# Kernel optimization log

Measured on AMD Instinct MI355X. Metric: run time of the kernel, lower is better.

Reference implementation:

```python
import jax, jax.numpy as jnp
import numpy as np

N = 20000      # nodes
E = 320000     # edges (before self-loops)
IN = 128       # in_channels
D = 256        # hidden_channels (d_model)
H = 8          # nhead
DH = D // H    # d_head
L = 2          # num_layers
B = 64         # NUM_DEGREE_BUCKETS
DFF = 2 * D    # dim_ff = d*2 per source


def setup_inputs() -> dict:
    key = jax.random.key(0)
    ks = jax.random.split(key, 24)
    w = lambda k, s: (jax.random.normal(k, s, jnp.float32) * 0.02)
    x = jax.random.normal(ks[0], (N, IN), jnp.float32)
    row = jax.random.randint(ks[1], (E,), 0, N, jnp.int32)
    col = jax.random.randint(ks[2], (E,), 0, N, jnp.int32)
    deg_emb = w(ks[3], (B, D)).at[0].set(0.0)  # padding_idx=0
    return dict(
        x=x, row=row, col=col,
        Wx=w(ks[4], (IN, D)), bx=jnp.zeros((D,), jnp.float32),
        deg_emb=deg_emb,
        sb=w(ks[5], (L, B, H)),
        Wq=w(ks[6], (L, D, D)), bq=jnp.zeros((L, D), jnp.float32),
        Wk=w(ks[7], (L, D, D)), bk=jnp.zeros((L, D), jnp.float32),
        Wv=w(ks[8], (L, D, D)), bv=jnp.zeros((L, D), jnp.float32),
        Wo=w(ks[9], (L, D, D)), bo=jnp.zeros((L, D), jnp.float32),
        ln1_g=jnp.ones((L, D), jnp.float32), ln1_b=jnp.zeros((L, D), jnp.float32),
        ln2_g=jnp.ones((L, D), jnp.float32), ln2_b=jnp.zeros((L, D), jnp.float32),
        W1=w(ks[10], (L, D, DFF)), b1=jnp.zeros((L, DFF), jnp.float32),
        W2=w(ks[11], (L, DFF, D)), b2=jnp.zeros((L, D), jnp.float32),
    )


def _ln(x, g, b):
    m = x.mean(-1, keepdims=True)
    v = ((x - m) ** 2).mean(-1, keepdims=True)
    return (x - m) / jnp.sqrt(v + 1e-5) * g + b


def reference(x, row, col, Wx, bx, deg_emb, sb, Wq, bq, Wk, bk, Wv, bv, Wo, bo,
              ln1_g, ln1_b, ln2_g, ln2_b, W1, b1, W2, b2):
    n = x.shape[0]
    # degree from original adjacency (before self loops)
    deg = jax.ops.segment_sum(jnp.ones_like(row, jnp.float32), row, num_segments=n)
    bucket = jnp.clip(jnp.floor(jnp.log2(jnp.maximum(deg, 1.0))), 1, B - 1).astype(jnp.int32)
    h = x @ Wx + bx + deg_emb[bucket]
    # set_diag(): append self loops
    sl = jnp.arange(n, dtype=row.dtype)
    r = jnp.concatenate([row, sl])
    c = jnp.concatenate([col, sl])
    scale = DH ** -0.5
    for i in range(L):
        Q = (h @ Wq[i] + bq[i]).reshape(n, H, DH)
        K = (h @ Wk[i] + bk[i]).reshape(n, H, DH)
        V = (h @ Wv[i] + bv[i]).reshape(n, H, DH)
        # per-edge multi-head scores + degree-bucket spatial bias  [E_tot, H]
        scores = (Q[r] * K[c]).sum(-1) * scale + sb[i][bucket[r]] + sb[i][bucket[c]]
        mx = jax.ops.segment_max(scores, r, num_segments=n)
        es = jnp.exp(scores - mx[r])
        ss = jax.ops.segment_sum(es, r, num_segments=n)
        alpha = es / jnp.maximum(ss[r], 1e-12)
        agg = jax.ops.segment_sum(alpha[:, :, None] * V[c], r, num_segments=n).reshape(n, D)
        out = agg @ Wo[i] + bo[i]
        h = _ln(h + out, ln1_g[i], ln1_b[i])
        ff = jax.nn.gelu(h @ W1[i] + b1[i], approximate=False) @ W2[i] + b2[i]
        h = _ln(h + ff, ln2_g[i], ln2_b[i])
    return h
```

## Files before the change

kernel.cpp:

```cpp
#include <hip/hip_runtime.h>
#include <hip/hip_bf16.h>
#include <math.h>

#define NNODES 20000
#define NPAD   20096
#define NEDGES 320000
#define INC 128
#define DMODEL 256
#define NHEAD 8
#define DHEAD 32
#define NLAYER 2
#define NBUCKET 64
#define DFF 512
#define ETOT (NEDGES + NNODES)
#define UNR 8

typedef __attribute__((ext_vector_type(8))) short short8v;
typedef __attribute__((ext_vector_type(4))) float f32x4;

__device__ __forceinline__ float bf2f(unsigned short u) {
    return __uint_as_float(((unsigned int)u) << 16);
}
__device__ __forceinline__ unsigned short f2bf(float f) {
    unsigned int u = __float_as_uint(f);
    unsigned int r = (u + 0x7FFFu + ((u >> 16) & 1u)) >> 16;
    return (unsigned short)r;
}
__device__ __forceinline__ void gl16(const unsigned short* g, unsigned short* l) {
    __builtin_amdgcn_global_load_lds(
        (const __attribute__((address_space(1))) void*)g,
        (__attribute__((address_space(3))) void*)l, 16, 0, 0);
}

__global__ void count_deg_k(const int* __restrict__ row, int* __restrict__ deg, int E) {
    int e = blockIdx.x * 256 + threadIdx.x;
    if (e < E) atomicAdd(&deg[row[e]], 1);
}

__global__ __launch_bounds__(1024) void scan_offsets_k(const int* __restrict__ deg,
                                                       int* __restrict__ off,
                                                       int* __restrict__ cur,
                                                       int* __restrict__ bkt, int n) {
    const int T = 1024;
    int t = threadIdx.x;
    int chunk = (n + T - 1) / T;
    int base = t * chunk;
    int s = 0;
    for (int i = 0; i < chunk; ++i) {
        int idx = base + i;
        if (idx < n) {
            int d = deg[idx];
            int dd = d < 1 ? 1 : d;
            int b = 31 - __clz(dd);
            bkt[idx] = min(max(b, 1), NBUCKET - 1);
            s += d + 1;
        }
    }
    __shared__ int ps[1024];
    ps[t] = s;
    __syncthreads();
    for (int d = 1; d < T; d <<= 1) {
        int v = (t >= d) ? ps[t - d] : 0;
        __syncthreads();
        ps[t] += v;
        __syncthreads();
    }
    int run = (t == 0) ? 0 : ps[t - 1];
    for (int i = 0; i < chunk; ++i) {
        int idx = base + i;
        if (idx < n) {
            off[idx] = run; cur[idx] = run;
            run += deg[idx] + 1;
        }
    }
    if (t == T - 1) off[n] = ps[T - 1];
}

__global__ void csr_fill_k(const int* __restrict__ row, const int* __restrict__ col,
                           const int* __restrict__ bkt,
                           int* __restrict__ cur, int* __restrict__ csr, int E, int n) {
    int e = blockIdx.x * 256 + threadIdx.x;
    if (e < E) {
        int c = col[e];
        int p = atomicAdd(&cur[row[e]], 1);
        csr[p] = c | (bkt[c] << 19);
    } else if (e < E + n) {
        int nn = e - E;
        int p = atomicAdd(&cur[nn], 1);
        csr[p] = nn | (bkt[nn] << 19);
    }
}

__global__ void cvt_bf16_k(const float* __restrict__ s, unsigned short* __restrict__ d, int n) {
    int i = (blockIdx.x * 256 + threadIdx.x) * 4;
    if (i < n) {
        float4 v = *(const float4*)(s + i);
        ushort4 o;
        o.x = f2bf(v.x); o.y = f2bf(v.y); o.z = f2bf(v.z); o.w = f2bf(v.w);
        *(ushort4*)(d + i) = o;
    }
}

struct TDesc { const float* src; unsigned short* dst; int K; int N; int tileStart; };
struct TPack { TDesc d[13]; int nd; };

__global__ __launch_bounds__(256) void mega_transpose_k(TPack p) {
    __shared__ float tile[32][33];
    const int tb = blockIdx.x;
    int di = 0;
    for (int i = 1; i < 13; ++i)
        if (i < p.nd && p.d[i].tileStart <= tb) di = i;
    const float* __restrict__ src = p.d[di].src;
    unsigned short* __restrict__ dst = p.d[di].dst;
    const int K = p.d[di].K, N = p.d[di].N;
    const int local = tb - p.d[di].tileStart;
    const int tpn = N >> 5;
    const int n0 = (local % tpn) * 32;
    const int k0 = (local / tpn) * 32;
    const int t = threadIdx.x;
    {
        int r = t >> 3, c = (t & 7) * 4;
        float4 v = *(const float4*)(src + (size_t)(k0 + r) * N + n0 + c);
        tile[r][c] = v.x; tile[r][c + 1] = v.y; tile[r][c + 2] = v.z; tile[r][c + 3] = v.w;
    }
    __syncthreads();
    {
        int n = t >> 3, k = (t & 7) * 4;
        ushort4 o;
        o.x = f2bf(tile[k][n]); o.y = f2bf(tile[k + 1][n]);
        o.z = f2bf(tile[k + 2][n]); o.w = f2bf(tile[k + 3][n]);
        *(ushort4*)(dst + (size_t)(n0 + n) * K + k0 + k) = o;
    }
}

__global__ void concat_bias2_k(const float* __restrict__ bq, const float* __restrict__ bk,
                               const float* __restrict__ bv,
                               float* __restrict__ d0, float* __restrict__ d1) {
    int t = blockIdx.x * 256 + threadIdx.x;
    int l = t / 768, u = t - l * 768;
    float v;
    if (u < 256) v = bq[l * DMODEL + u];
    else if (u < 512) v = bk[l * DMODEL + u - 256];
    else v = bv[l * DMODEL + u - 512];
    (l ? d1 : d0)[u] = v;
}

__global__ __launch_bounds__(256) void gemm_bf16_k(
        const unsigned short* __restrict__ A, const unsigned short* __restrict__ Wt,
        const float* __restrict__ bias,
        float* __restrict__ Cf, unsigned short* __restrict__ Cb,
        int M, int K, int Nout,
        const float* __restrict__ emb, const int* __restrict__ bkt, int act) {
    __shared__ unsigned short As[128 * 32];
    __shared__ unsigned short Bs[128 * 32];
    const int bm = blockIdx.x * 128;
    const int bn = blockIdx.y * 128;
    const int t = threadIdx.x;
    const int wid = t >> 6, lane = t & 63;
    const int wm = wid >> 1, wn = wid & 1;
    const int l16 = lane & 15, kslc = lane >> 4;
    const int srow = lane >> 2, scol = (lane & 3) * 8;

    f32x4 acc[4][4] = {};

    for (int k0 = 0; k0 < K; k0 += 32) {
        const unsigned short* gA = A + (size_t)(bm + wid * 32 + srow) * K + k0 + scol;
        const unsigned short* gB = Wt + (size_t)(bn + wid * 32 + srow) * K + k0 + scol;
        gl16(gA,          &As[(wid * 32) * 32]);
        gl16(gA + 16 * K, &As[(wid * 32 + 16) * 32]);
        gl16(gB,          &Bs[(wid * 32) * 32]);
        gl16(gB + 16 * K, &Bs[(wid * 32 + 16) * 32]);
        __syncthreads();
        short8v a[4], b[4];
        #pragma unroll
        for (int f = 0; f < 4; ++f) {
            a[f] = *(const short8v*)(&As[(wm * 64 + f * 16 + l16) * 32 + kslc * 8]);
            b[f] = *(const short8v*)(&Bs[(wn * 64 + f * 16 + l16) * 32 + kslc * 8]);
        }
        #pragma unroll
        for (int fm = 0; fm < 4; ++fm)
            #pragma unroll
            for (int fn = 0; fn < 4; ++fn)
                acc[fm][fn] = __builtin_amdgcn_mfma_f32_16x16x32_bf16(
                    a[fm], b[fn], acc[fm][fn], 0, 0, 0);
        __syncthreads();
    }

    #pragma unroll
    for (int fm = 0; fm < 4; ++fm) {
        #pragma unroll
        for (int fn = 0; fn < 4; ++fn) {
            int cc = wn * 64 + fn * 16 + l16;
            int gn = bn + cc;
            float bn_v = bias[gn];
            int rbase = bm + wm * 64 + fm * 16 + (lane >> 4) * 4;
            #pragma unroll
            for (int r = 0; r < 4; ++r) {
                int gm = rbase + r;
                if (gm >= M) continue;
                float v = acc[fm][fn][r] + bn_v;
                if (emb) v += emb[(size_t)bkt[gm] * Nout + gn];
                if (act) v = 0.5f * v * (1.f + erff(v * 0.70710678118654752f));
                if (Cf) Cf[(size_t)gm * Nout + gn] = v;
                if (Cb) Cb[(size_t)gm * Nout + gn] = f2bf(v);
            }
        }
    }
}


#define LOADB(CC, KK, VV, SB, J)                                               \
    do {                                                                        \
        _Pragma("unroll")                                                       \
        for (int e = 0; e < UNR; ++e)                                           \
            CC[e] = csr[min((J) + e, s1 - 1)];                                  \
        _Pragma("unroll")                                                       \
        for (int e = 0; e < UNR; ++e) {                                         \
            const unsigned short* base =                                        \
                QKV + (size_t)(CC[e] & 0x7FFFF) * 768 + hh * 32 + d2 * 2;       \
            KK[e] = *(const ushort2*)(base + 256);                              \
            VV[e] = *(const ushort2*)(base + 512);                              \
            SB[e] = sb_i[(CC[e] >> 19) * NHEAD + hh];                           \
        }                                                                       \
    } while (0)

#define COMPUTE(KK, VV, SB, J)                                                 \
    do {                                                                        \
        _Pragma("unroll")                                                       \
        for (int e = 0; e < UNR; ++e) {                                         \
            float p = qx * bf2f(KK[e].x) + qy * bf2f(KK[e].y);                  \
            _Pragma("unroll")                                                   \
            for (int mk = 8; mk >= 1; mk >>= 1) p += __shfl_xor(p, mk);         \
            float sc = p * scale + sbn + SB[e];                                 \
            if ((J) + e < s1) {                                                 \
                float mn = fmaxf(m, sc);                                        \
                float corr = __expf(m - mn);                                    \
                float es = __expf(sc - mn);                                     \
                s = s * corr + es;                                              \
                ax = ax * corr + es * bf2f(VV[e].x);                            \
                ay = ay * corr + es * bf2f(VV[e].y);                            \
                m = mn;                                                         \
            }                                                                   \
        }                                                                       \
    } while (0)

__global__ __launch_bounds__(128) void attn_bf16_k(
        const unsigned short* __restrict__ QKV,
        const int* __restrict__ off, const int* __restrict__ csr,
        const int* __restrict__ bkt, const float* __restrict__ sb_i,
        unsigned short* __restrict__ aggb) {
    const int node = blockIdx.x;
    const int t = threadIdx.x;
    const int hh = t >> 4, d2 = t & 15;
    const int s0 = off[node], s1 = off[node + 1];
    const ushort2 q2 = *(const ushort2*)(QKV + (size_t)node * 768 + hh * 32 + d2 * 2);
    const float qx = bf2f(q2.x), qy = bf2f(q2.y);
    const float sbn = sb_i[bkt[node] * NHEAD + hh];
    const float scale = 0.17677669529663689f;
    float m = -1e30f, s = 0.f, ax = 0.f, ay = 0.f;

    int ccA[UNR]; ushort2 kkA[UNR], vvA[UNR]; float sbA[UNR];
    int ccB[UNR]; ushort2 kkB[UNR], vvB[UNR]; float sbB[UNR];

    LOADB(ccA, kkA, vvA, sbA, s0);
    for (int j = s0; j < s1; j += 2 * UNR) {
        LOADB(ccB, kkB, vvB, sbB, j + UNR);
        COMPUTE(kkA, vvA, sbA, j);
        LOADB(ccA, kkA, vvA, sbA, j + 2 * UNR);
        COMPUTE(kkB, vvB, sbB, j + UNR);
    }

    float inv = 1.f / fmaxf(s, 1e-12f);
    ushort2 o;
    o.x = f2bf(ax * inv); o.y = f2bf(ay * inv);
    *(ushort2*)(aggb + (size_t)node * DMODEL + hh * 32 + d2 * 2) = o;
}

__global__ __launch_bounds__(256) void add_ln_k(float* __restrict__ h,
                                                const float* __restrict__ add,
                                                const float* __restrict__ g,
                                                const float* __restrict__ b,
                                                unsigned short* __restrict__ hb) {
    const int r = blockIdx.x;
    const int t = threadIdx.x;
    float x = h[(size_t)r * DMODEL + t] + add[(size_t)r * DMODEL + t];
    __shared__ float red[4];
    float s = x;
    #pragma unroll
    for (int mk = 32; mk >= 1; mk >>= 1) s += __shfl_xor(s, mk);
    if ((t & 63) == 0) red[t >> 6] = s;
    __syncthreads();
    float mean = (red[0] + red[1] + red[2] + red[3]) * (1.f / DMODEL);
    float dx = x - mean;
    __syncthreads();
    float v = dx * dx;
    #pragma unroll
    for (int mk = 32; mk >= 1; mk >>= 1) v += __shfl_xor(v, mk);
    if ((t & 63) == 0) red[t >> 6] = v;
    __syncthreads();
    float var = (red[0] + red[1] + red[2] + red[3]) * (1.f / DMODEL);
    float y = dx * rsqrtf(var + 1e-5f) * g[t] + b[t];
    h[(size_t)r * DMODEL + t] = y;
    hb[(size_t)r * DMODEL + t] = f2bf(y);
}

extern "C" void kernel_launch(void* const* d_in, const int* in_sizes, int n_in,
                              void* d_out, int out_size, void* d_ws, size_t ws_size,
                              hipStream_t stream) {
    const float* x      = (const float*)d_in[0];
    const int*   row    = (const int*)d_in[1];
    const int*   col    = (const int*)d_in[2];
    const float* Wx     = (const float*)d_in[3];
    const float* bx     = (const float*)d_in[4];
    const float* degemb = (const float*)d_in[5];
    const float* sb     = (const float*)d_in[6];
    const float* Wq     = (const float*)d_in[7];
    const float* bq     = (const float*)d_in[8];
    const float* Wk     = (const float*)d_in[9];
    const float* bk     = (const float*)d_in[10];
    const float* Wv     = (const float*)d_in[11];
    const float* bv     = (const float*)d_in[12];
    const float* Wo     = (const float*)d_in[13];
    const float* bo     = (const float*)d_in[14];
    const float* ln1g   = (const float*)d_in[15];
    const float* ln1b   = (const float*)d_in[16];
    const float* ln2g   = (const float*)d_in[17];
    const float* ln2b   = (const float*)d_in[18];
    const float* W1     = (const float*)d_in[19];
    const float* b1     = (const float*)d_in[20];
    const float* W2     = (const float*)d_in[21];
    const float* b2     = (const float*)d_in[22];

    const int Nn = NNODES, E = NEDGES;
    float* h = (float*)d_out;

    char* w = (char*)d_ws;
    unsigned short* hb   = (unsigned short*)w; w += (size_t)NPAD * DMODEL * 2;
    unsigned short* QKVb = (unsigned short*)w; w += (size_t)Nn * 768 * 2;
    unsigned short* AGGb = (unsigned short*)w; w += (size_t)NPAD * DMODEL * 2;
    unsigned short* FFb  = (unsigned short*)w; w += (size_t)NPAD * DFF * 2;
    float*          OUT  = (float*)w;          w += (size_t)Nn * DMODEL * 4;
    unsigned short* xb   = (unsigned short*)w; w += (size_t)NPAD * INC * 2;
    unsigned short* Wxt  = (unsigned short*)w; w += (size_t)DMODEL * INC * 2;
    unsigned short* Wqkvt[NLAYER]; float* bqkv[NLAYER];
    unsigned short *Wot[NLAYER], *W1t[NLAYER], *W2t[NLAYER];
    for (int l = 0; l < NLAYER; ++l) {
        Wqkvt[l] = (unsigned short*)w; w += (size_t)768 * DMODEL * 2;
        bqkv[l]  = (float*)w;          w += 768 * 4;
        Wot[l]   = (unsigned short*)w; w += (size_t)DMODEL * DMODEL * 2;
        W1t[l]   = (unsigned short*)w; w += (size_t)DFF * DMODEL * 2;
        W2t[l]   = (unsigned short*)w; w += (size_t)DMODEL * DFF * 2;
    }
    int* CSR = (int*)w; w += (size_t)ETOT * 4;
    int* OFF = (int*)w; w += (Nn + 1) * 4;
    int* CUR = (int*)w; w += Nn * 4;
    int* DEG = (int*)w; w += Nn * 4;
    int* BKT = (int*)w; w += Nn * 4;

    hipMemsetAsync(DEG, 0, Nn * sizeof(int), stream);
    count_deg_k<<<(E + 255) / 256, 256, 0, stream>>>(row, DEG, E);
    scan_offsets_k<<<1, 1024, 0, stream>>>(DEG, OFF, CUR, BKT, Nn);
    csr_fill_k<<<(E + Nn + 255) / 256, 256, 0, stream>>>(row, col, BKT, CUR, CSR, E, Nn);

    cvt_bf16_k<<<((size_t)Nn * INC / 4 + 255) / 256, 256, 0, stream>>>(x, xb, Nn * INC);
    {
        TPack pk; int nd = 0, tt = 0;
        auto add = [&](const float* s, unsigned short* d, int K, int N) {
            pk.d[nd].src = s; pk.d[nd].dst = d; pk.d[nd].K = K; pk.d[nd].N = N;
            pk.d[nd].tileStart = tt;
            tt += (K / 32) * (N / 32);
            ++nd;
        };
        const size_t DD = (size_t)DMODEL * DMODEL;
        add(Wx, Wxt, INC, DMODEL);
        for (int l = 0; l < NLAYER; ++l) {
            add(Wq + l * DD, Wqkvt[l],                DMODEL, DMODEL);
            add(Wk + l * DD, Wqkvt[l] + 256 * DMODEL, DMODEL, DMODEL);
            add(Wv + l * DD, Wqkvt[l] + 512 * DMODEL, DMODEL, DMODEL);
            add(Wo + l * DD, Wot[l], DMODEL, DMODEL);
            add(W1 + (size_t)l * DMODEL * DFF, W1t[l], DMODEL, DFF);
            add(W2 + (size_t)l * DFF * DMODEL, W2t[l], DFF, DMODEL);
        }
        pk.nd = nd;
        mega_transpose_k<<<tt, 256, 0, stream>>>(pk);
        concat_bias2_k<<<6, 256, 0, stream>>>(bq, bk, bv, bqkv[0], bqkv[1]);
    }

    const int MB = (Nn + 127) / 128;

    {
        dim3 grid(MB, DMODEL / 128);
        gemm_bf16_k<<<grid, 256, 0, stream>>>(xb, Wxt, bx, h, hb, Nn, INC, DMODEL,
                                              degemb, BKT, 0);
    }

    for (int l = 0; l < NLAYER; ++l) {
        const float* sb_i = sb + (size_t)l * NBUCKET * NHEAD;
        dim3 gQKV(MB, 768 / 128);
        dim3 gD(MB, DMODEL / 128);
        dim3 gF(MB, DFF / 128);

        gemm_bf16_k<<<gQKV, 256, 0, stream>>>(hb, Wqkvt[l], bqkv[l], nullptr, QKVb,
                                              Nn, DMODEL, 768, nullptr, nullptr, 0);
        attn_bf16_k<<<Nn, 128, 0, stream>>>(QKVb, OFF, CSR, BKT, sb_i, AGGb);
        gemm_bf16_k<<<gD, 256, 0, stream>>>(AGGb, Wot[l], bo + (size_t)l * DMODEL,
                                            OUT, nullptr, Nn, DMODEL, DMODEL,
                                            nullptr, nullptr, 0);
        add_ln_k<<<Nn, 256, 0, stream>>>(h, OUT, ln1g + (size_t)l * DMODEL,
                                         ln1b + (size_t)l * DMODEL, hb);
        gemm_bf16_k<<<gF, 256, 0, stream>>>(hb, W1t[l], b1 + (size_t)l * DFF,
                                            nullptr, FFb, Nn, DMODEL, DFF,
                                            nullptr, nullptr, 1);
        gemm_bf16_k<<<gD, 256, 0, stream>>>(FFb, W2t[l], b2 + (size_t)l * DMODEL,
                                            OUT, nullptr, Nn, DFF, DMODEL,
                                            nullptr, nullptr, 0);
        add_ln_k<<<Nn, 256, 0, stream>>>(h, OUT, ln2g + (size_t)l * DMODEL,
                                         ln2b + (size_t)l * DMODEL, hb);
    }
}
```

Measured before the change: 638.1 us.

## Fuse output and FFN2 GEMMs with residual add and LayerNorm

Adds a 512-thread GEMM kernel in which each block covers a 128-row by full 256-column tile, so the residual add and LayerNorm can be computed in the epilogue through shuffles and a shared-memory reduction. It replaces the separate N=256 GEMMs and the per-row add_ln kernels, removing the fp32 OUT intermediate buffer and four launches per forward. The cost is a grid of only about 157 blocks, each with a larger register footprint, which may leave the GPU underoccupied.

```diff
diff --git a/kernel.cpp b/kernel.cpp
--- a/kernel.cpp
+++ b/kernel.cpp
@@ -203,6 +203,146 @@
                 if (act) v = 0.5f * v * (1.f + erff(v * 0.70710678118654752f));
                 if (Cf) Cf[(size_t)gm * Nout + gn] = v;
                 if (Cb) Cb[(size_t)gm * Nout + gn] = f2bf(v);
+            }
+        }
+    }
+}
+
+__global__ __launch_bounds__(512) void gemm_ln_k(
+        const unsigned short* __restrict__ A, const unsigned short* __restrict__ Wt,
+        const float* __restrict__ bias,
+        float* __restrict__ h, unsigned short* __restrict__ hb,
+        const float* __restrict__ lng, const float* __restrict__ lnb,
+        int M, int K) {
+    __shared__ unsigned short As[128 * 32];
+    __shared__ unsigned short Bs[256 * 32];
+    __shared__ float red[128 * 4];
+    const int bm = blockIdx.x * 128;
+    const int t = threadIdx.x;
+    const int wid = t >> 6, lane = t & 63;
+    const int wm = wid >> 2, wn = wid & 3;
+    const int l16 = lane & 15, kslc = lane >> 4;
+    const int srow = lane >> 2, scol = (lane & 3) * 8;
+
+    f32x4 acc[4][4] = {};
+
+    for (int k0 = 0; k0 < K; k0 += 32) {
+        if (wid < 4) {
+            const unsigned short* gA = A + (size_t)(bm + wid * 32 + srow) * K + k0 + scol;
+            gl16(gA,          &As[(wid * 32) * 32]);
+            gl16(gA + 16 * K, &As[(wid * 32 + 16) * 32]);
+        } else {
+            const int w4 = wid - 4;
+            const unsigned short* gB = Wt + (size_t)(w4 * 64 + srow) * K + k0 + scol;
+            gl16(gB,          &Bs[(w4 * 64) * 32]);
+            gl16(gB + 16 * K, &Bs[(w4 * 64 + 16) * 32]);
+            gl16(gB + 32 * K, &Bs[(w4 * 64 + 32) * 32]);
+            gl16(gB + 48 * K, &Bs[(w4 * 64 + 48) * 32]);
+        }
+        __syncthreads();
+        short8v a[4], bb[4];
+        #pragma unroll
+        for (int f = 0; f < 4; ++f) {
+            a[f]  = *(const short8v*)(&As[(wm * 64 + f * 16 + l16) * 32 + kslc * 8]);
+            bb[f] = *(const short8v*)(&Bs[(wn * 64 + f * 16 + l16) * 32 + kslc * 8]);
+        }
+        #pragma unroll
+        for (int fm = 0; fm < 4; ++fm)
+            #pragma unroll
+            for (int fn = 0; fn < 4; ++fn)
+                acc[fm][fn] = __builtin_amdgcn_mfma_f32_16x16x32_bf16(
+                    a[fm], bb[fn], acc[fm][fn], 0, 0, 0);
+        __syncthreads();
+    }
+
+    #pragma unroll
+    for (int fm = 0; fm < 4; ++fm) {
+        #pragma unroll
+        for (int fn = 0; fn < 4; ++fn) {
+            const int gn = wn * 64 + fn * 16 + l16;
+            const float bv = bias[gn];
+            #pragma unroll
+            for (int r = 0; r < 4; ++r) {
+                const int gm = bm + wm * 64 + fm * 16 + kslc * 4 + r;
+                float v = acc[fm][fn][r] + bv;
+                if (gm < M) v += h[(size_t)gm * DMODEL + gn];
+                acc[fm][fn][r] = v;
+            }
+        }
+    }
+
+    float mean[4][4];
+    #pragma unroll
+    for (int fm = 0; fm < 4; ++fm)
+        #pragma unroll
+        for (int r = 0; r < 4; ++r) {
+            float p = acc[fm][0][r] + acc[fm][1][r] + acc[fm][2][r] + acc[fm][3][r];
+            #pragma unroll
+            for (int mk = 8; mk >= 1; mk >>= 1) p += __shfl_xor(p, mk);
+            mean[fm][r] = p;
+        }
+    if (l16 == 0) {
+        #pragma unroll
+        for (int fm = 0; fm < 4; ++fm)
+            #pragma unroll
+            for (int r = 0; r < 4; ++r)
+                red[(wm * 64 + fm * 16 + kslc * 4 + r) * 4 + wn] = mean[fm][r];
+    }
+    __syncthreads();
+    #pragma unroll
+    for (int fm = 0; fm < 4; ++fm)
+        #pragma unroll
+        for (int r = 0; r < 4; ++r) {
+            const int lr = wm * 64 + fm * 16 + kslc * 4 + r;
+            mean[fm][r] = (red[lr * 4] + red[lr * 4 + 1] + red[lr * 4 + 2] + red[lr * 4 + 3])
+                          * (1.f / DMODEL);
+        }
+    __syncthreads();
+
+    float var[4][4];
+    #pragma unroll
+    for (int fm = 0; fm < 4; ++fm)
+        #pragma unroll
+        for (int r = 0; r < 4; ++r) {
+            const float mu = mean[fm][r];
+            float d0 = acc[fm][0][r] - mu, d1 = acc[fm][1][r] - mu;
+            float d2 = acc[fm][2][r] - mu, d3 = acc[fm][3][r] - mu;
+            float p = d0 * d0 + d1 * d1 + d2 * d2 + d3 * d3;
+            #pragma unroll
+            for (int mk = 8; mk >= 1; mk >>= 1) p += __shfl_xor(p, mk);
+            var[fm][r] = p;
+        }
+    if (l16 == 0) {
+        #pragma unroll
+        for (int fm = 0; fm < 4; ++fm)
+            #pragma unroll
+            for (int r = 0; r < 4; ++r)
+                red[(wm * 64 + fm * 16 + kslc * 4 + r) * 4 + wn] = var[fm][r];
+    }
+    __syncthreads();
+    #pragma unroll
+    for (int fm = 0; fm < 4; ++fm)
+        #pragma unroll
+        for (int r = 0; r < 4; ++r) {
+            const int lr = wm * 64 + fm * 16 + kslc * 4 + r;
+            var[fm][r] = (red[lr * 4] + red[lr * 4 + 1] + red[lr * 4 + 2] + red[lr * 4 + 3])
+                         * (1.f / DMODEL);
+        }
+
+    #pragma unroll
+    for (int fm = 0; fm < 4; ++fm) {
+        #pragma unroll
+        for (int r = 0; r < 4; ++r) {
+            const int gm = bm + wm * 64 + fm * 16 + kslc * 4 + r;
+            if (gm >= M) continue;
+            const float mu = mean[fm][r];
+            const float rs = rsqrtf(var[fm][r] + 1e-5f);
+            #pragma unroll
+            for (int fn = 0; fn < 4; ++fn) {
+                const int gn = wn * 64 + fn * 16 + l16;
+                float y = (acc[fm][fn][r] - mu) * rs * lng[gn] + lnb[gn];
+                h[(size_t)gm * DMODEL + gn] = y;
+                hb[(size_t)gm * DMODEL + gn] = f2bf(y);
             }
         }
     }
@@ -274,34 +414,6 @@
     ushort2 o;
     o.x = f2bf(ax * inv); o.y = f2bf(ay * inv);
     *(ushort2*)(aggb + (size_t)node * DMODEL + hh * 32 + d2 * 2) = o;
-}
-
-__global__ __launch_bounds__(256) void add_ln_k(float* __restrict__ h,
-                                                const float* __restrict__ add,
-                                                const float* __restrict__ g,
-                                                const float* __restrict__ b,
-                                                unsigned short* __restrict__ hb) {
-    const int r = blockIdx.x;
-    const int t = threadIdx.x;
-    float x = h[(size_t)r * DMODEL + t] + add[(size_t)r * DMODEL + t];
-    __shared__ float red[4];
-    float s = x;
-    #pragma unroll
-    for (int mk = 32; mk >= 1; mk >>= 1) s += __shfl_xor(s, mk);
-    if ((t & 63) == 0) red[t >> 6] = s;
-    __syncthreads();
-    float mean = (red[0] + red[1] + red[2] + red[3]) * (1.f / DMODEL);
-    float dx = x - mean;
-    __syncthreads();
-    float v = dx * dx;
-    #pragma unroll
-    for (int mk = 32; mk >= 1; mk >>= 1) v += __shfl_xor(v, mk);
-    if ((t & 63) == 0) red[t >> 6] = v;
-    __syncthreads();
-    float var = (red[0] + red[1] + red[2] + red[3]) * (1.f / DMODEL);
-    float y = dx * rsqrtf(var + 1e-5f) * g[t] + b[t];
-    h[(size_t)r * DMODEL + t] = y;
-    hb[(size_t)r * DMODEL + t] = f2bf(y);
 }
 
 extern "C" void kernel_launch(void* const* d_in, const int* in_sizes, int n_in,
@@ -339,7 +451,6 @@
     unsigned short* QKVb = (unsigned short*)w; w += (size_t)Nn * 768 * 2;
     unsigned short* AGGb = (unsigned short*)w; w += (size_t)NPAD * DMODEL * 2;
     unsigned short* FFb  = (unsigned short*)w; w += (size_t)NPAD * DFF * 2;
-    float*          OUT  = (float*)w;          w += (size_t)Nn * DMODEL * 4;
     unsigned short* xb   = (unsigned short*)w; w += (size_t)NPAD * INC * 2;
     unsigned short* Wxt  = (unsigned short*)w; w += (size_t)DMODEL * INC * 2;
     unsigned short* Wqkvt[NLAYER]; float* bqkv[NLAYER];
@@ -397,24 +508,19 @@
     for (int l = 0; l < NLAYER; ++l) {
         const float* sb_i = sb + (size_t)l * NBUCKET * NHEAD;
         dim3 gQKV(MB, 768 / 128);
-        dim3 gD(MB, DMODEL / 128);
         dim3 gF(MB, DFF / 128);
 
         gemm_bf16_k<<<gQKV, 256, 0, stream>>>(hb, Wqkvt[l], bqkv[l], nullptr, QKVb,
                                               Nn, DMODEL, 768, nullptr, nullptr, 0);
         attn_bf16_k<<<Nn, 128, 0, stream>>>(QKVb, OFF, CSR, BKT, sb_i, AGGb);
-        gemm_bf16_k<<<gD, 256, 0, stream>>>(AGGb, Wot[l], bo + (size_t)l * DMODEL,
-                                            OUT, nullptr, Nn, DMODEL, DMODEL,
-                                            nullptr, nullptr, 0);
-        add_ln_k<<<Nn, 256, 0, stream>>>(h, OUT, ln1g + (size_t)l * DMODEL,
-                                         ln1b + (size_t)l * DMODEL, hb);
+        gemm_ln_k<<<MB, 512, 0, stream>>>(AGGb, Wot[l], bo + (size_t)l * DMODEL,
+                                          h, hb, ln1g + (size_t)l * DMODEL,
+                                          ln1b + (size_t)l * DMODEL, Nn, DMODEL);
         gemm_bf16_k<<<gF, 256, 0, stream>>>(hb, W1t[l], b1 + (size_t)l * DFF,
                                             nullptr, FFb, Nn, DMODEL, DFF,
                                             nullptr, nullptr, 1);
-        gemm_bf16_k<<<gD, 256, 0, stream>>>(FFb, W2t[l], b2 + (size_t)l * DMODEL,
-                                            OUT, nullptr, Nn, DFF, DMODEL,
-                                            nullptr, nullptr, 0);
-        add_ln_k<<<Nn, 256, 0, stream>>>(h, OUT, ln2g + (size_t)l * DMODEL,
-                                         ln2b + (size_t)l * DMODEL, hb);
-    }
-}
+        gemm_ln_k<<<MB, 512, 0, stream>>>(FFb, W2t[l], b2 + (size_t)l * DMODEL,
+                                          h, hb, ln2g + (size_t)l * DMODEL,
+                                          ln2b + (size_t)l * DMODEL, Nn, DFF);
+    }
+}
```

Result: no change. 632.8 us (-0.8%).
